# Optimization experiments

Measured on AMD Instinct MI355X. Metric: run time of the kernel, lower is better.

The kernel has to match this reference:

```python
import jax, jax.numpy as jnp
import numpy as np

K = 3  # hardcoded kNN size in the module

def setup_inputs() -> dict:
    key = jax.random.key(0)
    ks = jax.random.split(key, 8)
    B, M, N, C, NC, OUT = 2, 4096, 8192, 512, 20, 512
    def rn(k, sh, sc=1.0):
        return jax.random.normal(k, sh, dtype=jnp.float32) * sc
    return {
        "src_points": rn(ks[0], (B, M, 3)),
        "tgt_points": rn(ks[1], (B, N, 3)),
        "src_features": rn(ks[2], (B, M, C)),
        # semantic_head: Linear(C,128) -> ReLU -> Linear(128,NC)
        "w_sem1": rn(ks[3], (C, 128), 0.04), "b_sem1": jnp.zeros((128,), jnp.float32),
        "w_sem2": rn(ks[4], (128, NC), 0.08), "b_sem2": jnp.zeros((NC,), jnp.float32),
        # upsample_net: Linear(C+NC,256) -> ReLU -> Linear(256,OUT)
        "w_up1": rn(ks[5], (C + NC, 256), 0.04), "b_up1": jnp.zeros((256,), jnp.float32),
        "w_up2": rn(ks[6], (256, OUT), 0.06), "b_up2": jnp.zeros((OUT,), jnp.float32),
    }

def reference(src_points, tgt_points, src_features,
              w_sem1, b_sem1, w_sem2, b_sem2,
              w_up1, b_up1, w_up2, b_up2):
    # semantic logits per source point: [B, M, NC]
    semantic_logits = jax.nn.relu(src_features @ w_sem1 + b_sem1) @ w_sem2 + b_sem2
    # pairwise euclidean distances tgt->src: [B, N, M]
    d2 = (jnp.sum(tgt_points * tgt_points, -1)[:, :, None]
          + jnp.sum(src_points * src_points, -1)[:, None, :]
          - 2.0 * jnp.einsum('bnd,bmd->bnm', tgt_points, src_points))
    dists = jnp.sqrt(jnp.maximum(d2, 0.0))
    # k smallest distances and their indices
    neg_vals, knn_idx = jax.lax.top_k(-dists, K)   # [B, N, K]
    knn_d = -neg_vals                               # gathered distances, [B, N, K]
    # gather neighbor features / semantics: [B, N, K, C] and [B, N, K, NC]
    knn_features = jax.vmap(lambda f, i: f[i])(src_features, knn_idx)
    knn_semantic = jax.vmap(lambda f, i: f[i])(semantic_logits, knn_idx)
    # inverse-distance softmax weights over the K neighbors
    weights = jax.nn.softmax(-knn_d, axis=-1)                       # [B, N, K]
    semantic_weights = jax.nn.softmax(knn_semantic, axis=-1).mean(axis=2)  # [B, N, NC]
    fused_features = jnp.einsum('bnkd,bnk->bnd', knn_features, weights)    # [B, N, C]
    combined = jnp.concatenate([fused_features, semantic_weights], axis=-1)
    upsampled = jax.nn.relu(combined @ w_up1 + b_up1) @ w_up2 + b_up2      # [B, N, OUT]
    return (upsampled, semantic_logits)
```

## Files before the change

### kernel.cpp

```cpp
#include <hip/hip_runtime.h>
#include <math.h>

#define BB 2
#define MM 4096
#define NN 8192
#define CC 512
#define NC 20
#define OUTD 512
#define H1 128
#define H2 256
#define CIN 532
#define KNN 3
#define SPLIT 16
#define CHUNK (MM / SPLIT)
#define CLEN (CHUNK / 4)

#define RR 32
#define HS 264
#define KT1 17
#define KT2 8

#define RO 16
#define FS 520
#define HS2 136
#define TS 512
#define SKT1 16
#define SKT2 4

typedef __attribute__((ext_vector_type(8))) short s8;
typedef __attribute__((ext_vector_type(4))) float f4;

__device__ inline unsigned short f2bf(float x) {
    unsigned u = __float_as_uint(x);
    unsigned r = (u + 0x7FFFu + ((u >> 16) & 1u)) >> 16;
    return (unsigned short)r;
}
__device__ inline float bf2f(unsigned short u) {
    return __uint_as_float(((unsigned)u) << 16);
}
__device__ inline float bf2fs(short u) {
    return __uint_as_float(((unsigned)(unsigned short)u) << 16);
}

__global__ __launch_bounds__(256) void prep_kernel(
    const float* __restrict__ srcp,
    const float* __restrict__ wu1, const float* __restrict__ wu2,
    const float* __restrict__ ws1, const float* __restrict__ ws2,
    float4* __restrict__ sp4,
    unsigned short* __restrict__ w1p, unsigned short* __restrict__ w2p,
    unsigned short* __restrict__ ws1p, unsigned short* __restrict__ ws2p)
{
    int i = blockIdx.x * 256 + threadIdx.x;
    if (i < BB * MM) {
        float x = srcp[(size_t)i * 3 + 0];
        float y = srcp[(size_t)i * 3 + 1];
        float z = srcp[(size_t)i * 3 + 2];
        sp4[i] = make_float4(x, y, z, x * x + y * y + z * z);
    }
    if (i < KT1 * H2 * 32) {
        int kk = i & 31, n = (i >> 5) & 255, kb = i >> 13;
        int k = kb * 32 + kk;
        w1p[i] = f2bf((k < CIN) ? wu1[(size_t)k * H2 + n] : 0.0f);
    }
    if (i < KT2 * OUTD * 32) {
        int kk = i & 31, n = (i >> 5) & 511, kb = i >> 14;
        int k = kb * 32 + kk;
        w2p[i] = f2bf(wu2[(size_t)k * OUTD + n]);
    }
    if (i < SKT1 * H1 * 32) {
        int kk = i & 31, n = (i >> 5) & 127, kb = i >> 12;
        int k = kb * 32 + kk;
        ws1p[i] = f2bf(ws1[(size_t)k * H1 + n]);
    }
    if (i < SKT2 * 32 * 32) {
        int kk = i & 31, n = (i >> 5) & 31, kb = i >> 10;
        int k = kb * 32 + kk;
        ws2p[i] = f2bf((n < NC) ? ws2[(size_t)k * NC + n] : 0.0f);
    }
}

__global__ __launch_bounds__(256) void sem_kernel(
    const float* __restrict__ feat,
    const unsigned short* __restrict__ ws1p, const unsigned short* __restrict__ ws2p,
    const unsigned short* __restrict__ w1p,
    const float* __restrict__ b1s, const float* __restrict__ b2s,
    float* __restrict__ logits_out, unsigned short* __restrict__ T)
{
    __shared__ unsigned short sfeat[RO * FS];
    __shared__ unsigned short Tst[RO * TS];
    __shared__ unsigned short shid[RO * HS2];
    __shared__ float slg[RO][33];
    __shared__ unsigned short pP[RO * 32];
    const int tid = threadIdx.x;
    const int row0 = blockIdx.x * RO;
    const int lane = tid & 63;
    const int wv = tid >> 6;
    const int l15 = lane & 15;
    const int quad = lane >> 4;

    {
        const int r = tid >> 4, p = tid & 15;
        const float4* fr = (const float4*)(feat + (size_t)(row0 + r) * CC);
#pragma unroll
        for (int j = 0; j < 8; ++j) {
            int c4 = j * 16 + p;
            float4 a = fr[c4];
            ushort4 s;
            s.x = f2bf(a.x); s.y = f2bf(a.y); s.z = f2bf(a.z); s.w = f2bf(a.w);
            *(ushort4*)&sfeat[r * FS + c4 * 4] = s;
        }
    }
    __syncthreads();

    {
        f4 asem[2], ah[4];
#pragma unroll
        for (int c = 0; c < 2; ++c) asem[c] = (f4){0.f, 0.f, 0.f, 0.f};
#pragma unroll
        for (int c = 0; c < 4; ++c) ah[c] = (f4){0.f, 0.f, 0.f, 0.f};
        for (int kb = 0; kb < SKT1; ++kb) {
            s8 a = *(const s8*)&sfeat[l15 * FS + kb * 32 + quad * 8];
#pragma unroll
            for (int c = 0; c < 2; ++c) {
                s8 b = *(const s8*)&ws1p[((size_t)(kb * H1 + wv * 32 + c * 16 + l15)) * 32 + quad * 8];
                asem[c] = __builtin_amdgcn_mfma_f32_16x16x32_bf16(a, b, asem[c], 0, 0, 0);
            }
#pragma unroll
            for (int c = 0; c < 4; ++c) {
                s8 b = *(const s8*)&w1p[((size_t)(kb * H2 + wv * 64 + c * 16 + l15)) * 32 + quad * 8];
                ah[c] = __builtin_amdgcn_mfma_f32_16x16x32_bf16(a, b, ah[c], 0, 0, 0);
            }
        }
#pragma unroll
        for (int c = 0; c < 2; ++c) {
            int col = wv * 32 + c * 16 + l15;
            float bias = b1s[col];
#pragma unroll
            for (int i = 0; i < 4; ++i) {
                int rr = quad * 4 + i;
                shid[rr * HS2 + col] = f2bf(fmaxf(asem[c][i] + bias, 0.0f));
            }
        }
#pragma unroll
        for (int c = 0; c < 4; ++c) {
            int col = wv * 64 + c * 16 + l15;
#pragma unroll
            for (int i = 0; i < 4; ++i) {
                int rr = quad * 4 + i;
                Tst[rr * TS + col] = f2bf(ah[c][i]);
            }
        }
    }
    __syncthreads();

    if (wv < 2) {
        f4 acc = (f4){0.f, 0.f, 0.f, 0.f};
        for (int kb = 0; kb < SKT2; ++kb) {
            s8 a = *(const s8*)&shid[l15 * HS2 + kb * 32 + quad * 8];
            s8 b = *(const s8*)&ws2p[((size_t)(kb * 32 + wv * 16 + l15)) * 32 + quad * 8];
            acc = __builtin_amdgcn_mfma_f32_16x16x32_bf16(a, b, acc, 0, 0, 0);
        }
        int col = wv * 16 + l15;
        float bias = (col < NC) ? b2s[col] : 0.0f;
#pragma unroll
        for (int i = 0; i < 4; ++i) {
            int rr = quad * 4 + i;
            float v = acc[i] + bias;
            slg[rr][col] = v;
            if (col < NC)
                logits_out[(size_t)(row0 + rr) * NC + col] = v;
        }
    }
    __syncthreads();

    if (tid < RO) {
        int r = tid;
        float mx = -1e30f;
        for (int nc = 0; nc < NC; ++nc) mx = fmaxf(mx, slg[r][nc]);
        float s = 0.0f;
        float e[NC];
#pragma unroll
        for (int nc = 0; nc < NC; ++nc) { e[nc] = __expf(slg[r][nc] - mx); s += e[nc]; }
        float inv = 1.0f / s;
#pragma unroll
        for (int nc = 0; nc < 32; ++nc)
            pP[r * 32 + nc] = (nc < NC) ? f2bf(e[nc] * inv) : 0;
    }
    __syncthreads();

    {
        s8 a = *(const s8*)&pP[l15 * 32 + quad * 8];
#pragma unroll
        for (int c = 0; c < 4; ++c) {
            s8 b = *(const s8*)&w1p[((size_t)(16 * H2 + wv * 64 + c * 16 + l15)) * 32 + quad * 8];
            f4 acc = (f4){0.f, 0.f, 0.f, 0.f};
            acc = __builtin_amdgcn_mfma_f32_16x16x32_bf16(a, b, acc, 0, 0, 0);
            int col = wv * 64 + c * 16 + l15;
#pragma unroll
            for (int i = 0; i < 4; ++i) {
                int rr = quad * 4 + i;
                Tst[rr * TS + 256 + col] = f2bf(acc[i]);
            }
        }
    }
    __syncthreads();

    {
#pragma unroll
        for (int v = 0; v < 4; ++v) {
            int e = (tid + v * 256) * 8;
            int r = e >> 9, c = e & (TS - 1);
            s8 d = *(const s8*)&Tst[e];
            *(s8*)&T[((size_t)(row0 + r)) * TS + c] = d;
        }
    }
}

__global__ __launch_bounds__(256) void knn_partial(
    const float4* __restrict__ sp4, const float* __restrict__ tgtp,
    float* __restrict__ pd2, unsigned short* __restrict__ pidx)
{
    __shared__ float4 pts[CHUNK];
    const int tid = threadIdx.x;
    const int t = blockIdx.x * 256 + tid;
    const int bu = blockIdx.x >> 5;
    const int chunk = blockIdx.y;
    const int mbase = chunk * CHUNK;
    const float4* sp = sp4 + (size_t)bu * MM + mbase;
    pts[tid] = sp[tid];
    __syncthreads();

    const float tx = tgtp[(size_t)t * 3 + 0];
    const float ty = tgtp[(size_t)t * 3 + 1];
    const float tz = tgtp[(size_t)t * 3 + 2];
    const float m2x = -2.0f * tx, m2y = -2.0f * ty, m2z = -2.0f * tz;

    float b0[4], b1[4], b2[4];
    int i0[4], i1[4], i2[4];
#pragma unroll
    for (int k = 0; k < 4; ++k) {
        b0[k] = b1[k] = b2[k] = 1e30f;
        i0[k] = i1[k] = i2[k] = 0;
    }

#pragma unroll 2
    for (int m = 0; m < CLEN; ++m) {
#pragma unroll
        for (int k = 0; k < 4; ++k) {
            float4 p = pts[k * CLEN + m];
            float d = fmaf(m2x, p.x, fmaf(m2y, p.y, fmaf(m2z, p.z, p.w)));
            int mi = mbase + k * CLEN + m;
            bool l2 = d < b2[k], l1 = d < b1[k], l0 = d < b0[k];
            b2[k] = l1 ? b1[k] : (l2 ? d : b2[k]); i2[k] = l1 ? i1[k] : (l2 ? mi : i2[k]);
            b1[k] = l0 ? b0[k] : (l1 ? d : b1[k]); i1[k] = l0 ? i0[k] : (l1 ? mi : i1[k]);
            b0[k] = l0 ? d : b0[k];                i0[k] = l0 ? mi : i0[k];
        }
    }
#pragma unroll
    for (int k = 1; k < 4; ++k) {
#pragma unroll
        for (int j = 0; j < 3; ++j) {
            float d = (j == 0) ? b0[k] : (j == 1) ? b1[k] : b2[k];
            int   i = (j == 0) ? i0[k] : (j == 1) ? i1[k] : i2[k];
            bool e2 = d < b2[0], e1 = d < b1[0], e0 = d < b0[0];
            b2[0] = e1 ? b1[0] : (e2 ? d : b2[0]); i2[0] = e1 ? i1[0] : (e2 ? i : i2[0]);
            b1[0] = e0 ? b0[0] : (e1 ? d : b1[0]); i1[0] = e0 ? i0[0] : (e1 ? i : i1[0]);
            b0[0] = e0 ? d : b0[0];                i0[0] = e0 ? i : i0[0];
        }
    }
    size_t o = ((size_t)t * SPLIT + chunk) * KNN;
    pd2[o + 0] = b0[0]; pd2[o + 1] = b1[0]; pd2[o + 2] = b2[0];
    pidx[o + 0] = (unsigned short)i0[0];
    pidx[o + 1] = (unsigned short)i1[0];
    pidx[o + 2] = (unsigned short)i2[0];
}

__global__ __launch_bounds__(256) void up_kernel(
    const unsigned short* __restrict__ T,
    const float* __restrict__ pd2, const unsigned short* __restrict__ pidx,
    const float* __restrict__ tgtp,
    const unsigned short* __restrict__ w2p,
    const float* __restrict__ b1g, const float* __restrict__ b2g,
    float* __restrict__ out)
{
    __shared__ unsigned short hid[RR * HS];
    __shared__ float sg[RR][3];
    __shared__ int   sj[RR][3];
    const int tid = threadIdx.x;
    const int row0 = blockIdx.x * RR;
    const int lane = tid & 63;
    const int wv = tid >> 6;
    const int l15 = lane & 15;
    const int quad = lane >> 4;

    if (tid < RR) {
        int row = row0 + tid;
        float b0 = 1e30f, b1 = 1e30f, b2 = 1e30f;
        int i0 = 0, i1 = 0, i2 = 0;
        size_t base = (size_t)row * SPLIT * KNN;
#pragma unroll
        for (int j = 0; j < SPLIT * KNN; ++j) {
            float d = pd2[base + j];
            int m = pidx[base + j];
            bool l2 = d < b2, l1 = d < b1, l0 = d < b0;
            b2 = l1 ? b1 : (l2 ? d : b2); i2 = l1 ? i1 : (l2 ? m : i2);
            b1 = l0 ? b0 : (l1 ? d : b1); i1 = l0 ? i0 : (l1 ? m : i1);
            b0 = l0 ? d : b0;             i0 = l0 ? m : i0;
        }
        float tx = tgtp[(size_t)row * 3 + 0];
        float ty = tgtp[(size_t)row * 3 + 1];
        float tz = tgtp[(size_t)row * 3 + 2];
        float t2 = tx * tx + ty * ty + tz * tz;
        float d0 = sqrtf(fmaxf(b0 + t2, 0.0f));
        float d1 = sqrtf(fmaxf(b1 + t2, 0.0f));
        float d2v = sqrtf(fmaxf(b2 + t2, 0.0f));
        float e1 = __expf(d0 - d1);
        float e2 = __expf(d0 - d2v);
        float inv = 1.0f / (1.0f + e1 + e2);
        sg[tid][0] = inv; sg[tid][1] = e1 * inv; sg[tid][2] = e2 * inv;
        sj[tid][0] = i0; sj[tid][1] = i1; sj[tid][2] = i2;
    }
    __syncthreads();

    {
        const int r = tid >> 3, p = tid & 7, c0 = p * 32;
        int row = row0 + r;
        size_t bofs = (size_t)(row >> 13) * MM;
        float pre[32];
#pragma unroll
        for (int cc = 0; cc < 32; ++cc) pre[cc] = 0.0f;
#pragma unroll
        for (int k = 0; k < 3; ++k) {
            const unsigned short* Tr = T + (bofs + (size_t)sj[r][k]) * TS;
            float gk = sg[r][k];
#pragma unroll
            for (int v = 0; v < 4; ++v) {
                s8 h = *(const s8*)&Tr[c0 + v * 8];
                s8 g = *(const s8*)&Tr[256 + c0 + v * 8];
#pragma unroll
                for (int e = 0; e < 8; ++e) {
                    pre[v * 8 + e] = fmaf(gk, bf2fs(h[e]), pre[v * 8 + e]);
                    pre[v * 8 + e] = fmaf(1.0f / 3.0f, bf2fs(g[e]), pre[v * 8 + e]);
                }
            }
        }
#pragma unroll
        for (int cc = 0; cc < 32; ++cc) {
            int c = c0 + cc;
            hid[r * HS + c] = f2bf(fmaxf(pre[cc] + b1g[c], 0.0f));
        }
    }
    __syncthreads();

    {
        const int m0 = wv * 128;
        f4 acc2[2][8];
#pragma unroll
        for (int rt = 0; rt < 2; ++rt)
#pragma unroll
            for (int c = 0; c < 8; ++c) acc2[rt][c] = (f4){0.f, 0.f, 0.f, 0.f};
        for (int kb = 0; kb < KT2; ++kb) {
            s8 a0 = *(const s8*)&hid[l15 * HS + kb * 32 + quad * 8];
            s8 a1 = *(const s8*)&hid[(l15 + 16) * HS + kb * 32 + quad * 8];
            s8 bfr[8];
#pragma unroll
            for (int c = 0; c < 8; ++c)
                bfr[c] = *(const s8*)&w2p[((size_t)(kb * OUTD + m0 + c * 16 + l15)) * 32 + quad * 8];
#pragma unroll
            for (int c = 0; c < 8; ++c) {
                acc2[0][c] = __builtin_amdgcn_mfma_f32_16x16x32_bf16(a0, bfr[c], acc2[0][c], 0, 0, 0);
                acc2[1][c] = __builtin_amdgcn_mfma_f32_16x16x32_bf16(a1, bfr[c], acc2[1][c], 0, 0, 0);
            }
        }
#pragma unroll
        for (int c = 0; c < 8; ++c) {
            int ccol = m0 + c * 16 + l15;
            float bias = b2g[ccol];
#pragma unroll
            for (int rt = 0; rt < 2; ++rt)
#pragma unroll
                for (int i = 0; i < 4; ++i) {
                    int rr = rt * 16 + quad * 4 + i;
                    out[(size_t)(row0 + rr) * OUTD + ccol] = acc2[rt][c][i] + bias;
                }
        }
    }
}

extern "C" void kernel_launch(void* const* d_in, const int* in_sizes, int n_in,
                              void* d_out, int out_size, void* d_ws, size_t ws_size,
                              hipStream_t stream) {
    (void)in_sizes; (void)n_in; (void)out_size; (void)ws_size;
    const float* src_points   = (const float*)d_in[0];
    const float* tgt_points   = (const float*)d_in[1];
    const float* src_features = (const float*)d_in[2];
    const float* w_sem1 = (const float*)d_in[3];
    const float* b_sem1 = (const float*)d_in[4];
    const float* w_sem2 = (const float*)d_in[5];
    const float* b_sem2 = (const float*)d_in[6];
    const float* w_up1  = (const float*)d_in[7];
    const float* b_up1  = (const float*)d_in[8];
    const float* w_up2  = (const float*)d_in[9];
    const float* b_up2  = (const float*)d_in[10];

    float* out    = (float*)d_out;
    float* ups    = out;
    float* logits = out + (size_t)BB * NN * OUTD;

    char* w = (char*)d_ws;
    float4* sp4 = (float4*)w;                  w += (size_t)BB * MM * 16;
    unsigned short* T = (unsigned short*)w;    w += (size_t)BB * MM * TS * 2;
    float* pd2  = (float*)w;                   w += (size_t)BB * NN * SPLIT * KNN * 4;
    unsigned short* pidx = (unsigned short*)w; w += (size_t)BB * NN * SPLIT * KNN * 2;
    unsigned short* w1p  = (unsigned short*)w; w += (size_t)KT1 * H2 * 32 * 2;
    unsigned short* w2p  = (unsigned short*)w; w += (size_t)KT2 * OUTD * 32 * 2;
    unsigned short* ws1p = (unsigned short*)w; w += (size_t)SKT1 * H1 * 32 * 2;
    unsigned short* ws2p = (unsigned short*)w; w += (size_t)SKT2 * 32 * 32 * 2;

    prep_kernel<<<dim3((KT1 * H2 * 32 + 255) / 256), dim3(256), 0, stream>>>(
        src_points, w_up1, w_up2, w_sem1, w_sem2, sp4, w1p, w2p, ws1p, ws2p);
    sem_kernel<<<dim3(BB * MM / RO), dim3(256), 0, stream>>>(
        src_features, ws1p, ws2p, w1p, b_sem1, b_sem2, logits, T);
    knn_partial<<<dim3(BB * NN / 256, SPLIT), dim3(256), 0, stream>>>(
        sp4, tgt_points, pd2, pidx);
    up_kernel<<<dim3(BB * NN / RR), dim3(256), 0, stream>>>(
        T, pd2, pidx, tgt_points, w2p, b_up1, b_up2, ups);
}
```

Measured before the change: 168.7 us.

## Merge semantic MLP and kNN partial kernels into one heterogeneous launch

Combines the semantic-head/T-projection kernel and the kNN partial-search kernel into a single launch whose blocks branch on block index, so the two independent workloads can run concurrently on the GPU. Source-point packing (xyz plus squared norm) moves from the prep kernel into the kNN blocks, which removes the sp4 workspace buffer. This drops a kernel launch and boundary and lets the low-occupancy kNN and MFMA work overlap. In exchange, every block now reserves the larger shared-memory footprint, which can reduce occupancy for the kNN blocks, and the packing is recomputed per chunk.

```diff
diff --git a/kernel.cpp b/kernel.cpp
--- a/kernel.cpp
+++ b/kernel.cpp
@@ -17,8 +17,8 @@
 
 #define RR 32
 #define HS 264
+#define KT2 8
 #define KT1 17
-#define KT2 8
 
 #define RO 16
 #define FS 520
@@ -26,6 +26,8 @@
 #define TS 512
 #define SKT1 16
 #define SKT2 4
+#define NSEMB (BB * MM / RO)
+#define NKNNB (BB * NN / 256 * SPLIT)
 
 typedef __attribute__((ext_vector_type(8))) short s8;
 typedef __attribute__((ext_vector_type(4))) float f4;
@@ -35,28 +37,17 @@
     unsigned r = (u + 0x7FFFu + ((u >> 16) & 1u)) >> 16;
     return (unsigned short)r;
 }
-__device__ inline float bf2f(unsigned short u) {
-    return __uint_as_float(((unsigned)u) << 16);
-}
 __device__ inline float bf2fs(short u) {
     return __uint_as_float(((unsigned)(unsigned short)u) << 16);
 }
 
 __global__ __launch_bounds__(256) void prep_kernel(
-    const float* __restrict__ srcp,
     const float* __restrict__ wu1, const float* __restrict__ wu2,
     const float* __restrict__ ws1, const float* __restrict__ ws2,
-    float4* __restrict__ sp4,
     unsigned short* __restrict__ w1p, unsigned short* __restrict__ w2p,
     unsigned short* __restrict__ ws1p, unsigned short* __restrict__ ws2p)
 {
     int i = blockIdx.x * 256 + threadIdx.x;
-    if (i < BB * MM) {
-        float x = srcp[(size_t)i * 3 + 0];
-        float y = srcp[(size_t)i * 3 + 1];
-        float z = srcp[(size_t)i * 3 + 2];
-        sp4[i] = make_float4(x, y, z, x * x + y * y + z * z);
-    }
     if (i < KT1 * H2 * 32) {
         int kk = i & 31, n = (i >> 5) & 255, kb = i >> 13;
         int k = kb * 32 + kk;
@@ -79,200 +70,211 @@
     }
 }
 
-__global__ __launch_bounds__(256) void sem_kernel(
+__global__ __launch_bounds__(256) void phase1_kernel(
     const float* __restrict__ feat,
     const unsigned short* __restrict__ ws1p, const unsigned short* __restrict__ ws2p,
     const unsigned short* __restrict__ w1p,
     const float* __restrict__ b1s, const float* __restrict__ b2s,
-    float* __restrict__ logits_out, unsigned short* __restrict__ T)
+    float* __restrict__ logits_out, unsigned short* __restrict__ T,
+    const float* __restrict__ srcp, const float* __restrict__ tgtp,
+    float* __restrict__ pd2, unsigned short* __restrict__ pidx)
 {
-    __shared__ unsigned short sfeat[RO * FS];
-    __shared__ unsigned short Tst[RO * TS];
-    __shared__ unsigned short shid[RO * HS2];
-    __shared__ float slg[RO][33];
-    __shared__ unsigned short pP[RO * 32];
+    __shared__ __align__(16) char smem[40512];
     const int tid = threadIdx.x;
-    const int row0 = blockIdx.x * RO;
-    const int lane = tid & 63;
-    const int wv = tid >> 6;
-    const int l15 = lane & 15;
-    const int quad = lane >> 4;
-
-    {
-        const int r = tid >> 4, p = tid & 15;
-        const float4* fr = (const float4*)(feat + (size_t)(row0 + r) * CC);
-#pragma unroll
-        for (int j = 0; j < 8; ++j) {
-            int c4 = j * 16 + p;
-            float4 a = fr[c4];
-            ushort4 s;
-            s.x = f2bf(a.x); s.y = f2bf(a.y); s.z = f2bf(a.z); s.w = f2bf(a.w);
-            *(ushort4*)&sfeat[r * FS + c4 * 4] = s;
-        }
-    }
-    __syncthreads();
-
-    {
-        f4 asem[2], ah[4];
-#pragma unroll
-        for (int c = 0; c < 2; ++c) asem[c] = (f4){0.f, 0.f, 0.f, 0.f};
-#pragma unroll
-        for (int c = 0; c < 4; ++c) ah[c] = (f4){0.f, 0.f, 0.f, 0.f};
-        for (int kb = 0; kb < SKT1; ++kb) {
-            s8 a = *(const s8*)&sfeat[l15 * FS + kb * 32 + quad * 8];
+    const int bx = blockIdx.x;
+
+    if (bx < NSEMB) {
+        unsigned short* sfeat = (unsigned short*)smem;
+        unsigned short* Tst   = (unsigned short*)(smem + 16640);
+        unsigned short* shid  = (unsigned short*)(smem + 33024);
+        float*          slg   = (float*)(smem + 37376);
+        unsigned short* pP    = (unsigned short*)(smem + 39488);
+        const int row0 = bx * RO;
+        const int lane = tid & 63;
+        const int wv = tid >> 6;
+        const int l15 = lane & 15;
+        const int quad = lane >> 4;
+
+        {
+            const int r = tid >> 4, p = tid & 15;
+            const float4* fr = (const float4*)(feat + (size_t)(row0 + r) * CC);
+#pragma unroll
+            for (int j = 0; j < 8; ++j) {
+                int c4 = j * 16 + p;
+                float4 a = fr[c4];
+                ushort4 s;
+                s.x = f2bf(a.x); s.y = f2bf(a.y); s.z = f2bf(a.z); s.w = f2bf(a.w);
+                *(ushort4*)&sfeat[r * FS + c4 * 4] = s;
+            }
+        }
+        __syncthreads();
+
+        {
+            f4 asem[2], ah[4];
+#pragma unroll
+            for (int c = 0; c < 2; ++c) asem[c] = (f4){0.f, 0.f, 0.f, 0.f};
+#pragma unroll
+            for (int c = 0; c < 4; ++c) ah[c] = (f4){0.f, 0.f, 0.f, 0.f};
+            for (int kb = 0; kb < SKT1; ++kb) {
+                s8 a = *(const s8*)&sfeat[l15 * FS + kb * 32 + quad * 8];
+#pragma unroll
+                for (int c = 0; c < 2; ++c) {
+                    s8 b = *(const s8*)&ws1p[((size_t)(kb * H1 + wv * 32 + c * 16 + l15)) * 32 + quad * 8];
+                    asem[c] = __builtin_amdgcn_mfma_f32_16x16x32_bf16(a, b, asem[c], 0, 0, 0);
+                }
+#pragma unroll
+                for (int c = 0; c < 4; ++c) {
+                    s8 b = *(const s8*)&w1p[((size_t)(kb * H2 + wv * 64 + c * 16 + l15)) * 32 + quad * 8];
+                    ah[c] = __builtin_amdgcn_mfma_f32_16x16x32_bf16(a, b, ah[c], 0, 0, 0);
+                }
+            }
 #pragma unroll
             for (int c = 0; c < 2; ++c) {
-                s8 b = *(const s8*)&ws1p[((size_t)(kb * H1 + wv * 32 + c * 16 + l15)) * 32 + quad * 8];
-                asem[c] = __builtin_amdgcn_mfma_f32_16x16x32_bf16(a, b, asem[c], 0, 0, 0);
+                int col = wv * 32 + c * 16 + l15;
+                float bias = b1s[col];
+#pragma unroll
+                for (int i = 0; i < 4; ++i) {
+                    int rr = quad * 4 + i;
+                    shid[rr * HS2 + col] = f2bf(fmaxf(asem[c][i] + bias, 0.0f));
+                }
             }
 #pragma unroll
             for (int c = 0; c < 4; ++c) {
-                s8 b = *(const s8*)&w1p[((size_t)(kb * H2 + wv * 64 + c * 16 + l15)) * 32 + quad * 8];
-                ah[c] = __builtin_amdgcn_mfma_f32_16x16x32_bf16(a, b, ah[c], 0, 0, 0);
-            }
-        }
-#pragma unroll
-        for (int c = 0; c < 2; ++c) {
-            int col = wv * 32 + c * 16 + l15;
-            float bias = b1s[col];
+                int col = wv * 64 + c * 16 + l15;
+#pragma unroll
+                for (int i = 0; i < 4; ++i) {
+                    int rr = quad * 4 + i;
+                    Tst[rr * TS + col] = f2bf(ah[c][i]);
+                }
+            }
+        }
+        __syncthreads();
+
+        if (wv < 2) {
+            f4 acc = (f4){0.f, 0.f, 0.f, 0.f};
+            for (int kb = 0; kb < SKT2; ++kb) {
+                s8 a = *(const s8*)&shid[l15 * HS2 + kb * 32 + quad * 8];
+                s8 b = *(const s8*)&ws2p[((size_t)(kb * 32 + wv * 16 + l15)) * 32 + quad * 8];
+                acc = __builtin_amdgcn_mfma_f32_16x16x32_bf16(a, b, acc, 0, 0, 0);
+            }
+            int col = wv * 16 + l15;
+            float bias = (col < NC) ? b2s[col] : 0.0f;
 #pragma unroll
             for (int i = 0; i < 4; ++i) {
                 int rr = quad * 4 + i;
-                shid[rr * HS2 + col] = f2bf(fmaxf(asem[c][i] + bias, 0.0f));
-            }
-        }
-#pragma unroll
-        for (int c = 0; c < 4; ++c) {
-            int col = wv * 64 + c * 16 + l15;
-#pragma unroll
-            for (int i = 0; i < 4; ++i) {
-                int rr = quad * 4 + i;
-                Tst[rr * TS + col] = f2bf(ah[c][i]);
-            }
-        }
-    }
-    __syncthreads();
-
-    if (wv < 2) {
-        f4 acc = (f4){0.f, 0.f, 0.f, 0.f};
-        for (int kb = 0; kb < SKT2; ++kb) {
-            s8 a = *(const s8*)&shid[l15 * HS2 + kb * 32 + quad * 8];
-            s8 b = *(const s8*)&ws2p[((size_t)(kb * 32 + wv * 16 + l15)) * 32 + quad * 8];
-            acc = __builtin_amdgcn_mfma_f32_16x16x32_bf16(a, b, acc, 0, 0, 0);
-        }
-        int col = wv * 16 + l15;
-        float bias = (col < NC) ? b2s[col] : 0.0f;
-#pragma unroll
-        for (int i = 0; i < 4; ++i) {
-            int rr = quad * 4 + i;
-            float v = acc[i] + bias;
-            slg[rr][col] = v;
-            if (col < NC)
-                logits_out[(size_t)(row0 + rr) * NC + col] = v;
-        }
-    }
-    __syncthreads();
-
-    if (tid < RO) {
-        int r = tid;
-        float mx = -1e30f;
-        for (int nc = 0; nc < NC; ++nc) mx = fmaxf(mx, slg[r][nc]);
-        float s = 0.0f;
-        float e[NC];
-#pragma unroll
-        for (int nc = 0; nc < NC; ++nc) { e[nc] = __expf(slg[r][nc] - mx); s += e[nc]; }
-        float inv = 1.0f / s;
-#pragma unroll
-        for (int nc = 0; nc < 32; ++nc)
-            pP[r * 32 + nc] = (nc < NC) ? f2bf(e[nc] * inv) : 0;
-    }
-    __syncthreads();
-
-    {
-        s8 a = *(const s8*)&pP[l15 * 32 + quad * 8];
-#pragma unroll
-        for (int c = 0; c < 4; ++c) {
-            s8 b = *(const s8*)&w1p[((size_t)(16 * H2 + wv * 64 + c * 16 + l15)) * 32 + quad * 8];
-            f4 acc = (f4){0.f, 0.f, 0.f, 0.f};
-            acc = __builtin_amdgcn_mfma_f32_16x16x32_bf16(a, b, acc, 0, 0, 0);
-            int col = wv * 64 + c * 16 + l15;
-#pragma unroll
-            for (int i = 0; i < 4; ++i) {
-                int rr = quad * 4 + i;
-                Tst[rr * TS + 256 + col] = f2bf(acc[i]);
-            }
-        }
-    }
-    __syncthreads();
-
-    {
-#pragma unroll
-        for (int v = 0; v < 4; ++v) {
-            int e = (tid + v * 256) * 8;
-            int r = e >> 9, c = e & (TS - 1);
-            s8 d = *(const s8*)&Tst[e];
-            *(s8*)&T[((size_t)(row0 + r)) * TS + c] = d;
-        }
-    }
-}
-
-__global__ __launch_bounds__(256) void knn_partial(
-    const float4* __restrict__ sp4, const float* __restrict__ tgtp,
-    float* __restrict__ pd2, unsigned short* __restrict__ pidx)
-{
-    __shared__ float4 pts[CHUNK];
-    const int tid = threadIdx.x;
-    const int t = blockIdx.x * 256 + tid;
-    const int bu = blockIdx.x >> 5;
-    const int chunk = blockIdx.y;
-    const int mbase = chunk * CHUNK;
-    const float4* sp = sp4 + (size_t)bu * MM + mbase;
-    pts[tid] = sp[tid];
-    __syncthreads();
-
-    const float tx = tgtp[(size_t)t * 3 + 0];
-    const float ty = tgtp[(size_t)t * 3 + 1];
-    const float tz = tgtp[(size_t)t * 3 + 2];
-    const float m2x = -2.0f * tx, m2y = -2.0f * ty, m2z = -2.0f * tz;
-
-    float b0[4], b1[4], b2[4];
-    int i0[4], i1[4], i2[4];
-#pragma unroll
-    for (int k = 0; k < 4; ++k) {
-        b0[k] = b1[k] = b2[k] = 1e30f;
-        i0[k] = i1[k] = i2[k] = 0;
-    }
+                float v = acc[i] + bias;
+                slg[rr * 33 + col] = v;
+                if (col < NC)
+                    logits_out[(size_t)(row0 + rr) * NC + col] = v;
+            }
+        }
+        __syncthreads();
+
+        if (tid < RO) {
+            int r = tid;
+            float mx = -1e30f;
+            for (int nc = 0; nc < NC; ++nc) mx = fmaxf(mx, slg[r * 33 + nc]);
+            float s = 0.0f;
+            float e[NC];
+#pragma unroll
+            for (int nc = 0; nc < NC; ++nc) { e[nc] = __expf(slg[r * 33 + nc] - mx); s += e[nc]; }
+            float inv = 1.0f / s;
+#pragma unroll
+            for (int nc = 0; nc < 32; ++nc)
+                pP[r * 32 + nc] = (nc < NC) ? f2bf(e[nc] * inv) : 0;
+        }
+        __syncthreads();
+
+        {
+            const int lane2 = tid & 63, wv2 = tid >> 6;
+            const int l15b = lane2 & 15, quadb = lane2 >> 4;
+            s8 a = *(const s8*)&pP[l15b * 32 + quadb * 8];
+#pragma unroll
+            for (int c = 0; c < 4; ++c) {
+                s8 b = *(const s8*)&w1p[((size_t)(16 * H2 + wv2 * 64 + c * 16 + l15b)) * 32 + quadb * 8];
+                f4 acc = (f4){0.f, 0.f, 0.f, 0.f};
+                acc = __builtin_amdgcn_mfma_f32_16x16x32_bf16(a, b, acc, 0, 0, 0);
+                int col = wv2 * 64 + c * 16 + l15b;
+#pragma unroll
+                for (int i = 0; i < 4; ++i) {
+                    int rr = quadb * 4 + i;
+                    Tst[rr * TS + 256 + col] = f2bf(acc[i]);
+                }
+            }
+        }
+        __syncthreads();
+
+        {
+#pragma unroll
+            for (int v = 0; v < 4; ++v) {
+                int e = (tid + v * 256) * 8;
+                int r = e >> 9, c = e & (TS - 1);
+                s8 d = *(const s8*)&Tst[e];
+                *(s8*)&T[((size_t)(row0 + r)) * TS + c] = d;
+            }
+        }
+    } else {
+        float4* pts = (float4*)smem;
+        const int idx = bx - NSEMB;
+        const int g = idx & 63;
+        const int chunk = idx >> 6;
+        const int t = g * 256 + tid;
+        const int bu = g >> 5;
+        const int mbase = chunk * CHUNK;
+
+        {
+            const float* spg = srcp + ((size_t)bu * MM + mbase) * 3;
+            float x = spg[tid * 3 + 0];
+            float y = spg[tid * 3 + 1];
+            float z = spg[tid * 3 + 2];
+            pts[tid] = make_float4(x, y, z, x * x + y * y + z * z);
+        }
+        __syncthreads();
+
+        const float tx = tgtp[(size_t)t * 3 + 0];
+        const float ty = tgtp[(size_t)t * 3 + 1];
+        const float tz = tgtp[(size_t)t * 3 + 2];
+        const float m2x = -2.0f * tx, m2y = -2.0f * ty, m2z = -2.0f * tz;
+
+        float b0[4], b1[4], b2[4];
+        int i0[4], i1[4], i2[4];
+#pragma unroll
+        for (int k = 0; k < 4; ++k) {
+            b0[k] = b1[k] = b2[k] = 1e30f;
+            i0[k] = i1[k] = i2[k] = 0;
+        }
 
 #pragma unroll 2
-    for (int m = 0; m < CLEN; ++m) {
-#pragma unroll
-        for (int k = 0; k < 4; ++k) {
-            float4 p = pts[k * CLEN + m];
-            float d = fmaf(m2x, p.x, fmaf(m2y, p.y, fmaf(m2z, p.z, p.w)));
-            int mi = mbase + k * CLEN + m;
-            bool l2 = d < b2[k], l1 = d < b1[k], l0 = d < b0[k];
-            b2[k] = l1 ? b1[k] : (l2 ? d : b2[k]); i2[k] = l1 ? i1[k] : (l2 ? mi : i2[k]);
-            b1[k] = l0 ? b0[k] : (l1 ? d : b1[k]); i1[k] = l0 ? i0[k] : (l1 ? mi : i1[k]);
-            b0[k] = l0 ? d : b0[k];                i0[k] = l0 ? mi : i0[k];
-        }
-    }
-#pragma unroll
-    for (int k = 1; k < 4; ++k) {
-#pragma unroll
-        for (int j = 0; j < 3; ++j) {
-            float d = (j == 0) ? b0[k] : (j == 1) ? b1[k] : b2[k];
-            int   i = (j == 0) ? i0[k] : (j == 1) ? i1[k] : i2[k];
-            bool e2 = d < b2[0], e1 = d < b1[0], e0 = d < b0[0];
-            b2[0] = e1 ? b1[0] : (e2 ? d : b2[0]); i2[0] = e1 ? i1[0] : (e2 ? i : i2[0]);
-            b1[0] = e0 ? b0[0] : (e1 ? d : b1[0]); i1[0] = e0 ? i0[0] : (e1 ? i : i1[0]);
-            b0[0] = e0 ? d : b0[0];                i0[0] = e0 ? i : i0[0];
-        }
-    }
-    size_t o = ((size_t)t * SPLIT + chunk) * KNN;
-    pd2[o + 0] = b0[0]; pd2[o + 1] = b1[0]; pd2[o + 2] = b2[0];
-    pidx[o + 0] = (unsigned short)i0[0];
-    pidx[o + 1] = (unsigned short)i1[0];
-    pidx[o + 2] = (unsigned short)i2[0];
+        for (int m = 0; m < CLEN; ++m) {
+#pragma unroll
+            for (int k = 0; k < 4; ++k) {
+                float4 p = pts[k * CLEN + m];
+                float d = fmaf(m2x, p.x, fmaf(m2y, p.y, fmaf(m2z, p.z, p.w)));
+                int mi = mbase + k * CLEN + m;
+                bool l2 = d < b2[k], l1 = d < b1[k], l0 = d < b0[k];
+                b2[k] = l1 ? b1[k] : (l2 ? d : b2[k]); i2[k] = l1 ? i1[k] : (l2 ? mi : i2[k]);
+                b1[k] = l0 ? b0[k] : (l1 ? d : b1[k]); i1[k] = l0 ? i0[k] : (l1 ? mi : i1[k]);
+                b0[k] = l0 ? d : b0[k];                i0[k] = l0 ? mi : i0[k];
+            }
+        }
+#pragma unroll
+        for (int k = 1; k < 4; ++k) {
+#pragma unroll
+            for (int j = 0; j < 3; ++j) {
+                float d = (j == 0) ? b0[k] : (j == 1) ? b1[k] : b2[k];
+                int   i = (j == 0) ? i0[k] : (j == 1) ? i1[k] : i2[k];
+                bool e2 = d < b2[0], e1 = d < b1[0], e0 = d < b0[0];
+                b2[0] = e1 ? b1[0] : (e2 ? d : b2[0]); i2[0] = e1 ? i1[0] : (e2 ? i : i2[0]);
+                b1[0] = e0 ? b0[0] : (e1 ? d : b1[0]); i1[0] = e0 ? i0[0] : (e1 ? i : i1[0]);
+                b0[0] = e0 ? d : b0[0];                i0[0] = e0 ? i : i0[0];
+            }
+        }
+        size_t o = ((size_t)t * SPLIT + chunk) * KNN;
+        pd2[o + 0] = b0[0]; pd2[o + 1] = b1[0]; pd2[o + 2] = b2[0];
+        pidx[o + 0] = (unsigned short)i0[0];
+        pidx[o + 1] = (unsigned short)i1[0];
+        pidx[o + 2] = (unsigned short)i2[0];
+    }
 }
 
 __global__ __launch_bounds__(256) void up_kernel(
@@ -408,7 +410,6 @@
     float* logits = out + (size_t)BB * NN * OUTD;
 
     char* w = (char*)d_ws;
-    float4* sp4 = (float4*)w;                  w += (size_t)BB * MM * 16;
     unsigned short* T = (unsigned short*)w;    w += (size_t)BB * MM * TS * 2;
     float* pd2  = (float*)w;                   w += (size_t)BB * NN * SPLIT * KNN * 4;
     unsigned short* pidx = (unsigned short*)w; w += (size_t)BB * NN * SPLIT * KNN * 2;
@@ -418,11 +419,10 @@
     unsigned short* ws2p = (unsigned short*)w; w += (size_t)SKT2 * 32 * 32 * 2;
 
     prep_kernel<<<dim3((KT1 * H2 * 32 + 255) / 256), dim3(256), 0, stream>>>(
-        src_points, w_up1, w_up2, w_sem1, w_sem2, sp4, w1p, w2p, ws1p, ws2p);
-    sem_kernel<<<dim3(BB * MM / RO), dim3(256), 0, stream>>>(
-        src_features, ws1p, ws2p, w1p, b_sem1, b_sem2, logits, T);
-    knn_partial<<<dim3(BB * NN / 256, SPLIT), dim3(256), 0, stream>>>(
-        sp4, tgt_points, pd2, pidx);
+        w_up1, w_up2, w_sem1, w_sem2, w1p, w2p, ws1p, ws2p);
+    phase1_kernel<<<dim3(NSEMB + NKNNB), dim3(256), 0, stream>>>(
+        src_features, ws1p, ws2p, w1p, b_sem1, b_sem2, logits, T,
+        src_points, tgt_points, pd2, pidx);
     up_kernel<<<dim3(BB * NN / RR), dim3(256), 0, stream>>>(
         T, pd2, pidx, tgt_points, w2p, b_up1, b_up2, ups);
 }
```

Measured after the change: 162.5 us. 3.6% less time.
